# Optimization experiments

Measured on AMD Instinct MI355X. Metric: run time of the kernel, lower is better.

## Reference

```python
import jax, jax.numpy as jnp
import numpy as np
import math

B, L, H, E = 2, 2048, 16, 64  # S == L (self-attention, causal)

def setup_inputs() -> dict:
    key = jax.random.key(0)
    k1, k2, k3, k4, k5 = jax.random.split(key, 5)
    return {
        "queries": jax.random.normal(k1, (B, L, H, E), dtype=jnp.float32),
        "keys":    jax.random.normal(k2, (B, L, H, E), dtype=jnp.float32),
        "values":  jax.random.normal(k3, (B, L, H, E), dtype=jnp.float32),
        "w_score": jax.random.normal(k4, (2 * E,), dtype=jnp.float32),  # Linear(2E, 1) weight
        "b_score": jax.random.normal(k5, (1,), dtype=jnp.float32),      # Linear bias (scalar)
    }

def reference(queries, keys, values, w_score, b_score):
    # Linear over concat([q, k]) == <w_q, q> + <w_k, k> + b  (exactly the same math,
    # without materializing the [B,H,L,S,2E] broadcast tensor the torch code builds).
    Bq, Lq, Hq, Eq = queries.shape
    S = keys.shape[1]
    scale = 1.0 / math.sqrt(Eq)
    w_q, w_k = w_score[:Eq], w_score[Eq:]
    a_q = jnp.einsum("blhe,e->bhl", queries, w_q)  # [B,H,L]
    a_k = jnp.einsum("bshe,e->bhs", keys, w_k)     # [B,H,S]
    scores = (a_q[:, :, :, None] + a_k[:, :, None, :] + b_score[0]) * scale  # [B,H,L,S]
    # TriangularCausalMask: mask strictly-upper triangle (key index > query index)
    causal = jnp.triu(jnp.ones((Lq, S), dtype=bool), k=1)
    scores = jnp.where(causal[None, None], -jnp.inf, scores)
    weights = jax.nn.softmax(scores, axis=-1)  # dropout is identity in eval / p=0
    output = jnp.einsum("bhls,bshd->blhd", weights, values)  # [B,L,H,E]
    return output
```

## Files before the change

kernel.cpp:

```cpp
#include <hip/hip_runtime.h>
#include <math.h>

namespace {

constexpr int kB = 2, kL = 2048, kH = 16, kE = 64;
constexpr int kC  = 32;
constexpr int kNC = kL / kC;
constexpr int kBH = kB * kH;
constexpr int kRow = kH * kE;
constexpr float kScale = 0.125f;

constexpr size_t kUOff = 0;
constexpr size_t kTOff = (size_t)kBH * kL;
constexpr size_t kZOff = kTOff + (size_t)kBH * kNC * kE;

__global__ __launch_bounds__(64)
void phaseA(const float* __restrict__ keys, const float* __restrict__ values,
            const float* __restrict__ w_score, float* __restrict__ ws) {
  __shared__ float u_sh[kC];
  const int l  = threadIdx.x;
  const int c  = blockIdx.x & (kNC - 1);
  const int bh = blockIdx.x >> 6;
  const int b = bh >> 4, h = bh & 15;

  const int sl = l >> 1;
  const int eh = (l & 1) * 32;
  const int s0 = c * kC;
  const float4* kr = reinterpret_cast<const float4*>(
      keys + ((size_t)(b * kL + s0 + sl) * kRow + h * kE + eh));
  const float4* wv4 = reinterpret_cast<const float4*>(w_score + kE + eh);
  float ax = 0.f, ay = 0.f, az = 0.f, aw = 0.f;
#pragma unroll
  for (int j = 0; j < 8; ++j) {
    const float4 kv = kr[j];
    const float4 wv = wv4[j];
    ax = fmaf(kv.x, wv.x, ax);
    ay = fmaf(kv.y, wv.y, ay);
    az = fmaf(kv.z, wv.z, az);
    aw = fmaf(kv.w, wv.w, aw);
  }
  float p = (ax + ay) + (az + aw);
  p += __shfl_xor(p, 1);
  const float u = __expf(p * kScale);
  if (!(l & 1)) {
    u_sh[sl] = u;
    ws[kUOff + (size_t)bh * kL + s0 + sl] = u;
  }
  __syncthreads();

  float acc = 0.f, z = 0.f;
  const float* vp = values + ((size_t)(b * kL + s0) * kRow + h * kE) + l;
#pragma unroll
  for (int i = 0; i < kC; ++i) {
    const float us = u_sh[i];
    acc = fmaf(us, vp[(size_t)i * kRow], acc);
    z += us;
  }
  ws[kTOff + ((size_t)bh * kNC + c) * kE + l] = acc;
  if (l == 0) ws[kZOff + (size_t)bh * kNC + c] = z;
}

__global__ __launch_bounds__(64)
void phaseC(const float* __restrict__ values, const float* __restrict__ ws,
            float* __restrict__ out) {
  __shared__ float u_sh[kC];
  const int l  = threadIdx.x;
  const int c  = blockIdx.x & (kNC - 1);
  const int bh = blockIdx.x >> 6;
  const int b = bh >> 4, h = bh & 15;

  if (l < kC) u_sh[l] = ws[kUOff + (size_t)bh * kL + c * kC + l];

  const float* aggT = ws + kTOff + (size_t)bh * kNC * kE;
  float t0 = 0.f, t1 = 0.f, t2 = 0.f, t3 = 0.f,
        t4 = 0.f, t5 = 0.f, t6 = 0.f, t7 = 0.f;
  int j = 0;
  for (; j + 8 <= c; j += 8) {
    t0 += aggT[(size_t)(j + 0) * kE + l];
    t1 += aggT[(size_t)(j + 1) * kE + l];
    t2 += aggT[(size_t)(j + 2) * kE + l];
    t3 += aggT[(size_t)(j + 3) * kE + l];
    t4 += aggT[(size_t)(j + 4) * kE + l];
    t5 += aggT[(size_t)(j + 5) * kE + l];
    t6 += aggT[(size_t)(j + 6) * kE + l];
    t7 += aggT[(size_t)(j + 7) * kE + l];
  }
  for (; j < c; ++j) t0 += aggT[(size_t)j * kE + l];
  float acc = ((t0 + t1) + (t2 + t3)) + ((t4 + t5) + (t6 + t7));

  const float* aggZ = ws + kZOff + (size_t)bh * kNC;
  float zj = (l < c) ? aggZ[l] : 0.f;
#pragma unroll
  for (int m = 32; m; m >>= 1) zj += __shfl_xor(zj, m);
  float z = zj;

  __syncthreads();

  const size_t base = (size_t)(b * kL + c * kC) * kRow + h * kE + l;
  const float* vp = values + base;
  float* op = out + base;
#pragma unroll
  for (int i = 0; i < kC; ++i) {
    const float us = u_sh[i];
    acc = fmaf(us, vp[(size_t)i * kRow], acc);
    z += us;
    op[(size_t)i * kRow] = acc * __builtin_amdgcn_rcpf(z);
  }
}

}

extern "C" void kernel_launch(void* const* d_in, const int* in_sizes, int n_in,
                              void* d_out, int out_size, void* d_ws, size_t ws_size,
                              hipStream_t stream) {
  const float* keys    = (const float*)d_in[1];
  const float* values  = (const float*)d_in[2];
  const float* w_score = (const float*)d_in[3];
  float* out = (float*)d_out;
  float* ws  = (float*)d_ws;
  (void)d_in; (void)in_sizes; (void)n_in; (void)out_size; (void)ws_size;

  phaseA<<<kBH * kNC, 64, 0, stream>>>(keys, values, w_score, ws);
  phaseC<<<kBH * kNC, 64, 0, stream>>>(values, ws, out);
}
```

Baseline: 99.14 us.

## Pack four heads per block with float4 lanes in both phases

```diff
diff --git a/kernel.cpp b/kernel.cpp
--- a/kernel.cpp
+++ b/kernel.cpp
@@ -4,9 +4,10 @@
 namespace {
 
 constexpr int kB = 2, kL = 2048, kH = 16, kE = 64;
-constexpr int kC  = 32;
-constexpr int kNC = kL / kC;
-constexpr int kBH = kB * kH;
+constexpr int kC   = 32;
+constexpr int kNC  = kL / kC;
+constexpr int kBH  = kB * kH;
+constexpr int kHB  = 4;
 constexpr int kRow = kH * kE;
 constexpr float kScale = 0.125f;
 
@@ -14,97 +15,121 @@
 constexpr size_t kTOff = (size_t)kBH * kL;
 constexpr size_t kZOff = kTOff + (size_t)kBH * kNC * kE;
 
+
 __global__ __launch_bounds__(64)
 void phaseA(const float* __restrict__ keys, const float* __restrict__ values,
             const float* __restrict__ w_score, float* __restrict__ ws) {
-  __shared__ float u_sh[kC];
+  __shared__ float u_sh[kHB][kC + 1];
   const int l  = threadIdx.x;
-  const int c  = blockIdx.x & (kNC - 1);
-  const int bh = blockIdx.x >> 6;
-  const int b = bh >> 4, h = bh & 15;
+  const int hq = blockIdx.x & 3;
+  const int c  = (blockIdx.x >> 2) & 63;
+  const int b  = blockIdx.x >> 8;
+  const int hl = l >> 4;
+  const int h  = hq * kHB + hl;
+  const int g  = l & 15;
+  const int e4 = g * 4;
+  const int s0 = c * kC;
+  const int bh = b * kH + h;
 
-  const int sl = l >> 1;
-  const int eh = (l & 1) * 32;
-  const int s0 = c * kC;
-  const float4* kr = reinterpret_cast<const float4*>(
-      keys + ((size_t)(b * kL + s0 + sl) * kRow + h * kE + eh));
-  const float4* wv4 = reinterpret_cast<const float4*>(w_score + kE + eh);
-  float ax = 0.f, ay = 0.f, az = 0.f, aw = 0.f;
-#pragma unroll
-  for (int j = 0; j < 8; ++j) {
-    const float4 kv = kr[j];
-    const float4 wv = wv4[j];
-    ax = fmaf(kv.x, wv.x, ax);
-    ay = fmaf(kv.y, wv.y, ay);
-    az = fmaf(kv.z, wv.z, az);
-    aw = fmaf(kv.w, wv.w, aw);
-  }
-  float p = (ax + ay) + (az + aw);
-  p += __shfl_xor(p, 1);
-  const float u = __expf(p * kScale);
-  if (!(l & 1)) {
-    u_sh[sl] = u;
-    ws[kUOff + (size_t)bh * kL + s0 + sl] = u;
-  }
-  __syncthreads();
+  const float4 wv = *reinterpret_cast<const float4*>(w_score + kE + e4);
+  const float* kp = keys   + (size_t)(b * kL + s0) * kRow + h * kE + e4;
+  const float* vp = values + (size_t)(b * kL + s0) * kRow + h * kE + e4;
 
-  float acc = 0.f, z = 0.f;
-  const float* vp = values + ((size_t)(b * kL + s0) * kRow + h * kE) + l;
+  float a0 = 0.f, a1 = 0.f, a2 = 0.f, a3 = 0.f, z = 0.f;
 #pragma unroll
   for (int i = 0; i < kC; ++i) {
-    const float us = u_sh[i];
-    acc = fmaf(us, vp[(size_t)i * kRow], acc);
-    z += us;
+    const float4 kv = *reinterpret_cast<const float4*>(kp + (size_t)i * kRow);
+    float p = fmaf(kv.x, wv.x, fmaf(kv.y, wv.y, fmaf(kv.z, wv.z, kv.w * wv.w)));
+    p += __shfl_xor(p, 1);
+    p += __shfl_xor(p, 2);
+    p += __shfl_xor(p, 4);
+    p += __shfl_xor(p, 8);
+    const float u = __expf(p * kScale);
+    if (g == 0) u_sh[hl][i] = u;
+    const float4 vv = *reinterpret_cast<const float4*>(vp + (size_t)i * kRow);
+    a0 = fmaf(u, vv.x, a0);
+    a1 = fmaf(u, vv.y, a1);
+    a2 = fmaf(u, vv.z, a2);
+    a3 = fmaf(u, vv.w, a3);
+    z += u;
   }
-  ws[kTOff + ((size_t)bh * kNC + c) * kE + l] = acc;
-  if (l == 0) ws[kZOff + (size_t)bh * kNC + c] = z;
+
+  float* urow = ws + kUOff + (size_t)bh * kL + s0;
+  urow[g]      = u_sh[hl][g];
+  urow[16 + g] = u_sh[hl][16 + g];
+  float4* tdst = reinterpret_cast<float4*>(
+      ws + kTOff + ((size_t)bh * kNC + c) * kE + e4);
+  *tdst = make_float4(a0, a1, a2, a3);
+  if (g == 0) ws[kZOff + (size_t)bh * kNC + c] = z;
 }
 
 __global__ __launch_bounds__(64)
 void phaseC(const float* __restrict__ values, const float* __restrict__ ws,
             float* __restrict__ out) {
-  __shared__ float u_sh[kC];
+  __shared__ float u_sh[kHB][kC + 1];
   const int l  = threadIdx.x;
-  const int c  = blockIdx.x & (kNC - 1);
-  const int bh = blockIdx.x >> 6;
-  const int b = bh >> 4, h = bh & 15;
+  const int hq = blockIdx.x & 3;
+  const int c  = (blockIdx.x >> 2) & 63;
+  const int b  = blockIdx.x >> 8;
+  const int hl = l >> 4;
+  const int h  = hq * kHB + hl;
+  const int g  = l & 15;
+  const int e4 = g * 4;
+  const int s0 = c * kC;
+  const int bh = b * kH + h;
 
-  if (l < kC) u_sh[l] = ws[kUOff + (size_t)bh * kL + c * kC + l];
+  const float* urow = ws + kUOff + (size_t)bh * kL + s0;
+  u_sh[hl][g]      = urow[g];
+  u_sh[hl][16 + g] = urow[16 + g];
 
-  const float* aggT = ws + kTOff + (size_t)bh * kNC * kE;
-  float t0 = 0.f, t1 = 0.f, t2 = 0.f, t3 = 0.f,
-        t4 = 0.f, t5 = 0.f, t6 = 0.f, t7 = 0.f;
+  const float* aT = ws + kTOff + (size_t)bh * kNC * kE + e4;
+  float4 r0 = make_float4(0.f, 0.f, 0.f, 0.f), r1 = r0, r2 = r0, r3 = r0;
   int j = 0;
-  for (; j + 8 <= c; j += 8) {
-    t0 += aggT[(size_t)(j + 0) * kE + l];
-    t1 += aggT[(size_t)(j + 1) * kE + l];
-    t2 += aggT[(size_t)(j + 2) * kE + l];
-    t3 += aggT[(size_t)(j + 3) * kE + l];
-    t4 += aggT[(size_t)(j + 4) * kE + l];
-    t5 += aggT[(size_t)(j + 5) * kE + l];
-    t6 += aggT[(size_t)(j + 6) * kE + l];
-    t7 += aggT[(size_t)(j + 7) * kE + l];
+  for (; j + 4 <= c; j += 4) {
+    const float4 x0 = *reinterpret_cast<const float4*>(aT + (size_t)(j + 0) * kE);
+    const float4 x1 = *reinterpret_cast<const float4*>(aT + (size_t)(j + 1) * kE);
+    const float4 x2 = *reinterpret_cast<const float4*>(aT + (size_t)(j + 2) * kE);
+    const float4 x3 = *reinterpret_cast<const float4*>(aT + (size_t)(j + 3) * kE);
+    r0.x += x0.x; r0.y += x0.y; r0.z += x0.z; r0.w += x0.w;
+    r1.x += x1.x; r1.y += x1.y; r1.z += x1.z; r1.w += x1.w;
+    r2.x += x2.x; r2.y += x2.y; r2.z += x2.z; r2.w += x2.w;
+    r3.x += x3.x; r3.y += x3.y; r3.z += x3.z; r3.w += x3.w;
   }
-  for (; j < c; ++j) t0 += aggT[(size_t)j * kE + l];
-  float acc = ((t0 + t1) + (t2 + t3)) + ((t4 + t5) + (t6 + t7));
+  for (; j < c; ++j) {
+    const float4 x = *reinterpret_cast<const float4*>(aT + (size_t)j * kE);
+    r0.x += x.x; r0.y += x.y; r0.z += x.z; r0.w += x.w;
+  }
+  float4 acc;
+  acc.x = (r0.x + r1.x) + (r2.x + r3.x);
+  acc.y = (r0.y + r1.y) + (r2.y + r3.y);
+  acc.z = (r0.z + r1.z) + (r2.z + r3.z);
+  acc.w = (r0.w + r1.w) + (r2.w + r3.w);
 
-  const float* aggZ = ws + kZOff + (size_t)bh * kNC;
-  float zj = (l < c) ? aggZ[l] : 0.f;
-#pragma unroll
-  for (int m = 32; m; m >>= 1) zj += __shfl_xor(zj, m);
-  float z = zj;
+  const float* aZ = ws + kZOff + (size_t)bh * kNC;
+  float zp = 0.f;
+  for (int c2 = g; c2 < c; c2 += 16) zp += aZ[c2];
+  zp += __shfl_xor(zp, 1);
+  zp += __shfl_xor(zp, 2);
+  zp += __shfl_xor(zp, 4);
+  zp += __shfl_xor(zp, 8);
+  float z = zp;
 
-  __syncthreads();
-
-  const size_t base = (size_t)(b * kL + c * kC) * kRow + h * kE + l;
+  const size_t base = (size_t)(b * kL + s0) * kRow + h * kE + e4;
   const float* vp = values + base;
   float* op = out + base;
 #pragma unroll
   for (int i = 0; i < kC; ++i) {
-    const float us = u_sh[i];
-    acc = fmaf(us, vp[(size_t)i * kRow], acc);
+    const float us = u_sh[hl][i];
+    const float4 vv = *reinterpret_cast<const float4*>(vp + (size_t)i * kRow);
+    acc.x = fmaf(us, vv.x, acc.x);
+    acc.y = fmaf(us, vv.y, acc.y);
+    acc.z = fmaf(us, vv.z, acc.z);
+    acc.w = fmaf(us, vv.w, acc.w);
     z += us;
-    op[(size_t)i * kRow] = acc * __builtin_amdgcn_rcpf(z);
+    const float rz = __builtin_amdgcn_rcpf(z);
+    float4 o;
+    o.x = acc.x * rz; o.y = acc.y * rz; o.z = acc.z * rz; o.w = acc.w * rz;
+    *reinterpret_cast<float4*>(op + (size_t)i * kRow) = o;
   }
 }
 
@@ -120,6 +145,7 @@
   float* ws  = (float*)d_ws;
   (void)d_in; (void)in_sizes; (void)n_in; (void)out_size; (void)ws_size;
 
-  phaseA<<<kBH * kNC, 64, 0, stream>>>(keys, values, w_score, ws);
-  phaseC<<<kBH * kNC, 64, 0, stream>>>(values, ws, out);
+  const int grid = kB * (kL / kC) * (kH / kHB);
+  phaseA<<<grid, 64, 0, stream>>>(keys, values, w_score, ws);
+  phaseC<<<grid, 64, 0, stream>>>(values, ws, out);
 }
```

Measured after the change: 106.7 us. +7.6%, slower.

## Halve chunk size and prefetch value rows into registers before sync

Applied to the files above, without the earlier changes.

```diff
diff --git a/kernel.cpp b/kernel.cpp
--- a/kernel.cpp
+++ b/kernel.cpp
@@ -4,9 +4,9 @@
 namespace {
 
 constexpr int kB = 2, kL = 2048, kH = 16, kE = 64;
-constexpr int kC  = 32;
-constexpr int kNC = kL / kC;
-constexpr int kBH = kB * kH;
+constexpr int kC   = 16;
+constexpr int kNC  = kL / kC;
+constexpr int kBH  = kB * kH;
 constexpr int kRow = kH * kE;
 constexpr float kScale = 0.125f;
 
@@ -14,24 +14,25 @@
 constexpr size_t kTOff = (size_t)kBH * kL;
 constexpr size_t kZOff = kTOff + (size_t)kBH * kNC * kE;
 
+
 __global__ __launch_bounds__(64)
 void phaseA(const float* __restrict__ keys, const float* __restrict__ values,
             const float* __restrict__ w_score, float* __restrict__ ws) {
   __shared__ float u_sh[kC];
   const int l  = threadIdx.x;
   const int c  = blockIdx.x & (kNC - 1);
-  const int bh = blockIdx.x >> 6;
+  const int bh = blockIdx.x >> 7;
   const int b = bh >> 4, h = bh & 15;
+  const int s0 = c * kC;
 
-  const int sl = l >> 1;
-  const int eh = (l & 1) * 32;
-  const int s0 = c * kC;
+  const int sl = l >> 2;
+  const int eq = (l & 3) * 16;
   const float4* kr = reinterpret_cast<const float4*>(
-      keys + ((size_t)(b * kL + s0 + sl) * kRow + h * kE + eh));
-  const float4* wv4 = reinterpret_cast<const float4*>(w_score + kE + eh);
+      keys + ((size_t)(b * kL + s0 + sl) * kRow + h * kE + eq));
+  const float4* wv4 = reinterpret_cast<const float4*>(w_score + kE + eq);
   float ax = 0.f, ay = 0.f, az = 0.f, aw = 0.f;
 #pragma unroll
-  for (int j = 0; j < 8; ++j) {
+  for (int j = 0; j < 4; ++j) {
     const float4 kv = kr[j];
     const float4 wv = wv4[j];
     ax = fmaf(kv.x, wv.x, ax);
@@ -41,21 +42,25 @@
   }
   float p = (ax + ay) + (az + aw);
   p += __shfl_xor(p, 1);
+  p += __shfl_xor(p, 2);
   const float u = __expf(p * kScale);
-  if (!(l & 1)) {
-    u_sh[sl] = u;
-    ws[kUOff + (size_t)bh * kL + s0 + sl] = u;
-  }
+  if ((l & 3) == 0) u_sh[sl] = u;
+
+  const float* vp = values + ((size_t)(b * kL + s0) * kRow + h * kE) + l;
+  float vreg[kC];
+#pragma unroll
+  for (int i = 0; i < kC; ++i) vreg[i] = vp[(size_t)i * kRow];
   __syncthreads();
 
   float acc = 0.f, z = 0.f;
-  const float* vp = values + ((size_t)(b * kL + s0) * kRow + h * kE) + l;
 #pragma unroll
   for (int i = 0; i < kC; ++i) {
     const float us = u_sh[i];
-    acc = fmaf(us, vp[(size_t)i * kRow], acc);
+    acc = fmaf(us, vreg[i], acc);
     z += us;
   }
+
+  if (l < kC) ws[kUOff + (size_t)bh * kL + s0 + l] = u_sh[l];
   ws[kTOff + ((size_t)bh * kNC + c) * kE + l] = acc;
   if (l == 0) ws[kZOff + (size_t)bh * kNC + c] = z;
 }
@@ -66,10 +71,17 @@
   __shared__ float u_sh[kC];
   const int l  = threadIdx.x;
   const int c  = blockIdx.x & (kNC - 1);
-  const int bh = blockIdx.x >> 6;
+  const int bh = blockIdx.x >> 7;
   const int b = bh >> 4, h = bh & 15;
+  const int s0 = c * kC;
 
-  if (l < kC) u_sh[l] = ws[kUOff + (size_t)bh * kL + c * kC + l];
+  if (l < kC) u_sh[l] = ws[kUOff + (size_t)bh * kL + s0 + l];
+
+  const size_t base = (size_t)(b * kL + s0) * kRow + h * kE + l;
+  const float* vp = values + base;
+  float vreg[kC];
+#pragma unroll
+  for (int i = 0; i < kC; ++i) vreg[i] = vp[(size_t)i * kRow];
 
   const float* aggT = ws + kTOff + (size_t)bh * kNC * kE;
   float t0 = 0.f, t1 = 0.f, t2 = 0.f, t3 = 0.f,
@@ -89,20 +101,19 @@
   float acc = ((t0 + t1) + (t2 + t3)) + ((t4 + t5) + (t6 + t7));
 
   const float* aggZ = ws + kZOff + (size_t)bh * kNC;
-  float zj = (l < c) ? aggZ[l] : 0.f;
+  float zp = 0.f;
+  for (int c2 = l; c2 < c; c2 += 64) zp += aggZ[c2];
 #pragma unroll
-  for (int m = 32; m; m >>= 1) zj += __shfl_xor(zj, m);
-  float z = zj;
+  for (int m = 32; m; m >>= 1) zp += __shfl_xor(zp, m);
+  float z = zp;
 
   __syncthreads();
 
-  const size_t base = (size_t)(b * kL + c * kC) * kRow + h * kE + l;
-  const float* vp = values + base;
   float* op = out + base;
 #pragma unroll
   for (int i = 0; i < kC; ++i) {
     const float us = u_sh[i];
-    acc = fmaf(us, vp[(size_t)i * kRow], acc);
+    acc = fmaf(us, vreg[i], acc);
     z += us;
     op[(size_t)i * kRow] = acc * __builtin_amdgcn_rcpf(z);
   }
```

New measurement: 101.8 us. 2.7% more time.
